# Optimization experiments

Measured on AMD Instinct MI355X. Metric: run time of the kernel, lower is better.

The kernel has to match this reference:

```python
import jax, jax.numpy as jnp
import numpy as np

TAU = 1.0  # gumbel-softmax temperature (torch default arg temperature=1.0)
EPS = 1e-7


def setup_inputs() -> dict:
    key = jax.random.key(0)
    kx, kg, kc, kw = jax.random.split(key, 4)
    B, T, D = 8, 4096, 1024
    G, N = 2, 320
    Cd = D // G  # 512
    x = jax.random.normal(kx, (B, T, D), dtype=jnp.float32)
    # standard Gumbel(0,1) noise, same distribution torch samples internally
    u = jax.random.uniform(kg, (B, T, G, N), dtype=jnp.float32, minval=1e-6, maxval=1.0 - 1e-6)
    gumbel = -jnp.log(-jnp.log(u))
    # codebook init: uniform(-1/num_codes, 1/num_codes)
    codebook = jax.random.uniform(kc, (G, N, Cd), dtype=jnp.float32, minval=-1.0 / N, maxval=1.0 / N)
    proj_w = jax.random.normal(kw, (D, G * N), dtype=jnp.float32) * (1.0 / np.sqrt(D))
    proj_b = jnp.zeros((G * N,), dtype=jnp.float32)
    return {"x": x, "gumbel": gumbel, "codebook": codebook, "proj_w": proj_w, "proj_b": proj_b}


def reference(x, gumbel, codebook, proj_w, proj_b):
    B, T, D = x.shape
    G, N, Cd = codebook.shape
    # projection to per-group code logits: [B,T,G,N]
    logits = (jnp.einsum('btd,de->bte', x, proj_w) + proj_b).reshape(B, T, G, N)
    # hard gumbel-softmax with straight-through estimator (training path)
    y_soft = jax.nn.softmax((logits + gumbel) / TAU, axis=-1)
    idx = jnp.argmax(y_soft, axis=-1)                     # [B,T,G]
    y_hard = jax.nn.one_hot(idx, N, dtype=y_soft.dtype)   # [B,T,G,N]
    probs = y_hard - jax.lax.stop_gradient(y_soft) + y_soft
    # one-hot gather from codebook, expressed as the original einsum
    quantized = jnp.einsum('btgn,gnd->btgd', probs, codebook).reshape(B, T, D)
    # diversity loss: entropy of average code usage per group
    avg_probs = probs.mean(axis=(0, 1))                    # [G,N]
    diversity_loss = -jnp.sum(avg_probs * jnp.log(avg_probs + EPS)) / G
    return quantized, diversity_loss
```

## Files before the change

kernel.cpp:

```cpp
#include <hip/hip_runtime.h>
#include <math.h>

#define M_ROWS 32768
#define KDIM   1024
#define GN     640
#define NGRP   2
#define NCODES 320
#define CD     512

#define BM 64
#define BK 32
#define NT (KDIM / BK)
#define THREADS 512

#define B_TILE_BYTES (4 * GN * 16)

typedef __attribute__((ext_vector_type(8))) short bf16x8;
typedef __attribute__((ext_vector_type(4))) float f32x4;

__device__ __forceinline__ unsigned short f2bf(float f) {
    unsigned u = __builtin_bit_cast(unsigned, f);
    return (unsigned short)((u + 0x7FFFu + ((u >> 16) & 1u)) >> 16);
}
__device__ __forceinline__ unsigned pk2(float lo, float hi) {
    return (unsigned)f2bf(lo) | ((unsigned)f2bf(hi) << 16);
}

__device__ __forceinline__ void gll16(const void* g, void* l) {
    __builtin_amdgcn_global_load_lds(
        (const __attribute__((address_space(1))) unsigned int*)g,
        (__attribute__((address_space(3))) unsigned int*)l, 16, 0, 0);
}

__global__ __launch_bounds__(256) void wt2_kernel(const float* __restrict__ W,
                                                  unsigned short* __restrict__ Wt2,
                                                  int* __restrict__ counts) {
    const int k = blockIdx.x;
    const int t = k >> 5, ks = (k >> 3) & 3, j = k & 7;
    const size_t obase = (((size_t)t * 4 + ks) * GN) * 8 + j;
    for (int c = threadIdx.x; c < GN; c += 256)
        Wt2[obase + (size_t)c * 8] = f2bf(W[(size_t)k * GN + c]);
    if (k == 0)
        for (int i = threadIdx.x; i < GN; i += 256) counts[i] = 0;
}

__global__ __launch_bounds__(THREADS) void gemm_argmax_gather(
    const float* __restrict__ x,
    const float* __restrict__ gumbel,
    const float* __restrict__ codebook,
    const unsigned short* __restrict__ Wt2,
    const float* __restrict__ bias,
    float* __restrict__ out,
    int* __restrict__ counts)
{
    __shared__ __align__(16) unsigned short Bs[4][GN][8];
    __shared__ __align__(16) float As[BM][BK];
    __shared__ float pv[NGRP][2][BM];
    __shared__ int   pi[NGRP][2][BM];
    __shared__ int   idx_s[NGRP][BM];

    const int tid  = threadIdx.x;
    const int widx = tid >> 6;
    const int lane = tid & 63;
    const int l15  = lane & 15;
    const int l4   = lane >> 4;
    const int wn   = widx & 3;
    const int wm   = widx >> 2;
    const int row0 = blockIdx.x * BM;

    f32x4 acc[2][10];
#pragma unroll
    for (int mf = 0; mf < 2; ++mf)
#pragma unroll
        for (int nf = 0; nf < 10; ++nf) acc[mf][nf] = (f32x4){0.f, 0.f, 0.f, 0.f};

    const char* bsrc = (const char*)Wt2 + (size_t)(widx * 5) * 1024 + (size_t)lane * 16;
    char* BsBase = (char*)&Bs[0][0][0];
    const int arow = widx * 8 + (lane >> 3);
    const int asub = lane & 7;
    const int asg  = ((((asub >> 1) ^ (arow & 3)) << 1) | (asub & 1));
    const char* asrc = (const char*)x + (size_t)(row0 + arow) * (KDIM * 4) + (size_t)asg * 16;
    char* AsBase = (char*)&As[0][0];
    char* adst   = AsBase + widx * 1024;

#pragma unroll
    for (int i = 0; i < 5; ++i)
        gll16(bsrc + i * 1024, BsBase + (widx * 5 + i) * 1024);
    gll16(asrc, adst);
    __syncthreads();

    for (int t = 0; t < NT; ++t) {
        bf16x8 afr[2];
#pragma unroll
        for (int mf = 0; mf < 2; ++mf) {
            const int row = wm * 32 + mf * 16 + l15;
            const int q   = l4 ^ (row & 3);
            const float4* pa = reinterpret_cast<const float4*>(AsBase + row * 128 + q * 32);
            float4 a0 = pa[0], a1 = pa[1];
            union { bf16x8 v; unsigned u[4]; } w;
            w.u[0] = pk2(a0.x, a0.y); w.u[1] = pk2(a0.z, a0.w);
            w.u[2] = pk2(a1.x, a1.y); w.u[3] = pk2(a1.z, a1.w);
            afr[mf] = w.v;
        }
#pragma unroll
        for (int nf = 0; nf < 10; ++nf) {
            bf16x8 bfr = *reinterpret_cast<const bf16x8*>(
                BsBase + ((size_t)l4 * GN + wn * 160 + nf * 16 + l15) * 16);
            acc[0][nf] = __builtin_amdgcn_mfma_f32_16x16x32_bf16(afr[0], bfr, acc[0][nf], 0, 0, 0);
            acc[1][nf] = __builtin_amdgcn_mfma_f32_16x16x32_bf16(afr[1], bfr, acc[1][nf], 0, 0, 0);
        }
        __syncthreads();
        if (t + 1 < NT) {
#pragma unroll
            for (int i = 0; i < 5; ++i)
                gll16(bsrc + (size_t)(t + 1) * B_TILE_BYTES + i * 1024,
                      BsBase + (widx * 5 + i) * 1024);
            gll16(asrc + (size_t)(t + 1) * 128, adst);
        }
        __syncthreads();
    }

#pragma unroll
    for (int mf = 0; mf < 2; ++mf) {
#pragma unroll
        for (int j = 0; j < 4; ++j) {
            const int lr = wm * 32 + mf * 16 + l4 * 4 + j;
            const size_t grow = (size_t)(row0 + lr) * GN;
            float best = -INFINITY;
            int bidx = 0;
#pragma unroll
            for (int nf = 0; nf < 10; ++nf) {
                int c = wn * 160 + nf * 16 + l15;
                float v = acc[mf][nf][j] + bias[c] + gumbel[grow + c];
                if (v > best) { best = v; bidx = c; }
            }
#pragma unroll
            for (int m = 1; m < 16; m <<= 1) {
                float ov = __shfl_xor(best, m, 64);
                int   oi = __shfl_xor(bidx, m, 64);
                if (ov > best || (ov == best && oi < bidx)) { best = ov; bidx = oi; }
            }
            if (l15 == 0) {
                pv[wn >> 1][wn & 1][lr] = best;
                pi[wn >> 1][wn & 1][lr] = bidx;
            }
        }
    }
    __syncthreads();

    if (tid < NGRP * BM) {
        const int g = tid >> 6, lr = tid & 63;
        float v0 = pv[g][0][lr], v1 = pv[g][1][lr];
        int   i0 = pi[g][0][lr], i1 = pi[g][1][lr];
        int bi = (v1 > v0) ? i1 : i0;
        int n  = bi - g * NCODES;
        idx_s[g][lr] = n;
        atomicAdd(&counts[g * NCODES + n], 1);
    }
    __syncthreads();

#pragma unroll
    for (int s = 0; s < 32; ++s) {
        int fi = tid + THREADS * s;
        int lr = fi >> 8;
        int q  = fi & 255;
        int g  = q >> 7;
        int n  = idx_s[g][lr];
        float4 cv = *reinterpret_cast<const float4*>(
            &codebook[((size_t)g * NCODES + n) * CD + (q & 127) * 4]);
        *reinterpret_cast<float4*>(&out[(size_t)(row0 + lr) * KDIM + q * 4]) = cv;
    }
}

__global__ void loss_kernel(const int* __restrict__ counts, float* __restrict__ out_loss) {
    __shared__ float red[256];
    float sum = 0.0f;
    for (int i = threadIdx.x; i < GN; i += 256) {
        float avg = (float)counts[i] * (1.0f / (float)M_ROWS);
        sum += avg * logf(avg + 1e-7f);
    }
    red[threadIdx.x] = sum;
    __syncthreads();
    for (int s = 128; s > 0; s >>= 1) {
        if (threadIdx.x < s) red[threadIdx.x] += red[threadIdx.x + s];
        __syncthreads();
    }
    if (threadIdx.x == 0) out_loss[0] = -red[0] * (1.0f / (float)NGRP);
}

extern "C" void kernel_launch(void* const* d_in, const int* in_sizes, int n_in,
                              void* d_out, int out_size, void* d_ws, size_t ws_size,
                              hipStream_t stream) {
    const float* x        = (const float*)d_in[0];
    const float* gumbel   = (const float*)d_in[1];
    const float* codebook = (const float*)d_in[2];
    const float* W        = (const float*)d_in[3];
    const float* bias     = (const float*)d_in[4];
    float* out = (float*)d_out;

    unsigned short* Wt2 = (unsigned short*)d_ws;
    int* counts = (int*)((char*)d_ws + (size_t)GN * KDIM * 2 + 256);

    wt2_kernel<<<dim3(KDIM), dim3(256), 0, stream>>>(W, Wt2, counts);
    gemm_argmax_gather<<<dim3(M_ROWS / BM), dim3(THREADS), 0, stream>>>(
        x, gumbel, codebook, Wt2, bias, out, counts);
    loss_kernel<<<dim3(1), dim3(256), 0, stream>>>(
        counts, out + (size_t)M_ROWS * KDIM);
}
```

Baseline: 126.2 us.

## Split GEMM across column quarters with atomicMax argmax keys and separate gather

Each block now computes a 64-row by 160-column quarter of the logits instead of all 640 columns. The partial argmax results are combined through 64-bit atomicMax keys that pack an order-preserving float with an inverted index. The codebook gather and usage counting move into a separate kernel. The GEMM now double-buffers B in LDS, prefetches A straight into registers, and swizzles block IDs for XCD locality. The intent is more parallelism and lower per-block register/LDS use, at the cost of reading x four times, an extra kernel launch, and global atomics.

```diff
diff --git a/kernel.cpp b/kernel.cpp
--- a/kernel.cpp
+++ b/kernel.cpp
@@ -11,9 +11,10 @@
 #define BM 64
 #define BK 32
 #define NT (KDIM / BK)
-#define THREADS 512
-
-#define B_TILE_BYTES (4 * GN * 16)
+#define QBN 160
+#define NQ 4
+#define QSLAB 10240
+#define THREADS 256
 
 typedef __attribute__((ext_vector_type(8))) short bf16x8;
 typedef __attribute__((ext_vector_type(4))) float f32x4;
@@ -25,150 +26,148 @@
 __device__ __forceinline__ unsigned pk2(float lo, float hi) {
     return (unsigned)f2bf(lo) | ((unsigned)f2bf(hi) << 16);
 }
-
 __device__ __forceinline__ void gll16(const void* g, void* l) {
     __builtin_amdgcn_global_load_lds(
         (const __attribute__((address_space(1))) unsigned int*)g,
         (__attribute__((address_space(3))) unsigned int*)l, 16, 0, 0);
 }
 
-__global__ __launch_bounds__(256) void wt2_kernel(const float* __restrict__ W,
-                                                  unsigned short* __restrict__ Wt2,
-                                                  int* __restrict__ counts) {
+__global__ __launch_bounds__(256) void prep_kernel(const float* __restrict__ W,
+                                                   unsigned short* __restrict__ Wt3,
+                                                   unsigned long long* __restrict__ keys,
+                                                   int* __restrict__ counts) {
     const int k = blockIdx.x;
     const int t = k >> 5, ks = (k >> 3) & 3, j = k & 7;
-    const size_t obase = (((size_t)t * 4 + ks) * GN) * 8 + j;
-    for (int c = threadIdx.x; c < GN; c += 256)
-        Wt2[obase + (size_t)c * 8] = f2bf(W[(size_t)k * GN + c]);
-    if (k == 0)
+    for (int c = threadIdx.x; c < GN; c += 256) {
+        int qq = c / QBN, cl = c % QBN;
+        Wt3[((((size_t)t * NQ + qq) * 4 + ks) * QBN + cl) * 8 + j] =
+            f2bf(W[(size_t)k * GN + c]);
+    }
+    int gtid = blockIdx.x * 256 + threadIdx.x;
+    if (gtid < M_ROWS * NGRP) keys[gtid] = 0ull;
+    if (blockIdx.x == 0)
         for (int i = threadIdx.x; i < GN; i += 256) counts[i] = 0;
 }
 
-__global__ __launch_bounds__(THREADS) void gemm_argmax_gather(
+__global__ __launch_bounds__(THREADS) void gemm_argmax(
     const float* __restrict__ x,
     const float* __restrict__ gumbel,
-    const float* __restrict__ codebook,
-    const unsigned short* __restrict__ Wt2,
+    const unsigned short* __restrict__ Wt3,
     const float* __restrict__ bias,
-    float* __restrict__ out,
-    int* __restrict__ counts)
+    unsigned long long* __restrict__ keys)
 {
-    __shared__ __align__(16) unsigned short Bs[4][GN][8];
-    __shared__ __align__(16) float As[BM][BK];
-    __shared__ float pv[NGRP][2][BM];
-    __shared__ int   pi[NGRP][2][BM];
-    __shared__ int   idx_s[NGRP][BM];
+    __shared__ __align__(16) unsigned short Bs[2][4][QBN][8];
 
     const int tid  = threadIdx.x;
-    const int widx = tid >> 6;
+    const int wid  = tid >> 6;
     const int lane = tid & 63;
     const int l15  = lane & 15;
     const int l4   = lane >> 4;
-    const int wn   = widx & 3;
-    const int wm   = widx >> 2;
-    const int row0 = blockIdx.x * BM;
-
-    f32x4 acc[2][10];
-#pragma unroll
-    for (int mf = 0; mf < 2; ++mf)
-#pragma unroll
-        for (int nf = 0; nf < 10; ++nf) acc[mf][nf] = (f32x4){0.f, 0.f, 0.f, 0.f};
-
-    const char* bsrc = (const char*)Wt2 + (size_t)(widx * 5) * 1024 + (size_t)lane * 16;
-    char* BsBase = (char*)&Bs[0][0][0];
-    const int arow = widx * 8 + (lane >> 3);
-    const int asub = lane & 7;
-    const int asg  = ((((asub >> 1) ^ (arow & 3)) << 1) | (asub & 1));
-    const char* asrc = (const char*)x + (size_t)(row0 + arow) * (KDIM * 4) + (size_t)asg * 16;
-    char* AsBase = (char*)&As[0][0];
-    char* adst   = AsBase + widx * 1024;
-
-#pragma unroll
-    for (int i = 0; i < 5; ++i)
-        gll16(bsrc + i * 1024, BsBase + (widx * 5 + i) * 1024);
-    gll16(asrc, adst);
+
+    const int b   = blockIdx.x;
+    const int xcd = b & 7;
+    const int l   = b >> 3;
+    const int qq  = l & 3;
+    const int rt  = xcd * 64 + (l >> 2);
+    const int row0 = rt * BM;
+
+    f32x4 acc[10];
+#pragma unroll
+    for (int nf = 0; nf < 10; ++nf) acc[nf] = (f32x4){0.f, 0.f, 0.f, 0.f};
+
+    const float* aptr = x + (size_t)(row0 + wid * 16 + l15) * KDIM + l4 * 8;
+    const char* bsrc = (const char*)Wt3 + (size_t)qq * QSLAB + (size_t)lane * 16;
+    char* BsB = (char*)&Bs[0][0][0][0];
+
+    for (int s = wid; s < 10; s += 4)
+        gll16(bsrc + s * 1024, BsB + s * 1024);
+    float4 a0 = *reinterpret_cast<const float4*>(aptr);
+    float4 a1 = *reinterpret_cast<const float4*>(aptr + 4);
     __syncthreads();
 
     for (int t = 0; t < NT; ++t) {
-        bf16x8 afr[2];
-#pragma unroll
-        for (int mf = 0; mf < 2; ++mf) {
-            const int row = wm * 32 + mf * 16 + l15;
-            const int q   = l4 ^ (row & 3);
-            const float4* pa = reinterpret_cast<const float4*>(AsBase + row * 128 + q * 32);
-            float4 a0 = pa[0], a1 = pa[1];
-            union { bf16x8 v; unsigned u[4]; } w;
-            w.u[0] = pk2(a0.x, a0.y); w.u[1] = pk2(a0.z, a0.w);
-            w.u[2] = pk2(a1.x, a1.y); w.u[3] = pk2(a1.z, a1.w);
-            afr[mf] = w.v;
-        }
+        const int buf = t & 1;
+        float4 n0, n1;
+        if (t + 1 < NT) {
+            for (int s = wid; s < 10; s += 4)
+                gll16(bsrc + (size_t)(t + 1) * (NQ * QSLAB) + s * 1024,
+                      BsB + (buf ^ 1) * QSLAB + s * 1024);
+            n0 = *reinterpret_cast<const float4*>(aptr + (t + 1) * BK);
+            n1 = *reinterpret_cast<const float4*>(aptr + (t + 1) * BK + 4);
+        }
+        union { bf16x8 v; unsigned u[4]; } w;
+        w.u[0] = pk2(a0.x, a0.y); w.u[1] = pk2(a0.z, a0.w);
+        w.u[2] = pk2(a1.x, a1.y); w.u[3] = pk2(a1.z, a1.w);
+        bf16x8 af = w.v;
 #pragma unroll
         for (int nf = 0; nf < 10; ++nf) {
             bf16x8 bfr = *reinterpret_cast<const bf16x8*>(
-                BsBase + ((size_t)l4 * GN + wn * 160 + nf * 16 + l15) * 16);
-            acc[0][nf] = __builtin_amdgcn_mfma_f32_16x16x32_bf16(afr[0], bfr, acc[0][nf], 0, 0, 0);
-            acc[1][nf] = __builtin_amdgcn_mfma_f32_16x16x32_bf16(afr[1], bfr, acc[1][nf], 0, 0, 0);
-        }
+                BsB + buf * QSLAB + ((l4 * QBN + nf * 16 + l15) * 16));
+            acc[nf] = __builtin_amdgcn_mfma_f32_16x16x32_bf16(af, bfr, acc[nf], 0, 0, 0);
+        }
+        if (t + 1 < NT) { a0 = n0; a1 = n1; }
         __syncthreads();
-        if (t + 1 < NT) {
-#pragma unroll
-            for (int i = 0; i < 5; ++i)
-                gll16(bsrc + (size_t)(t + 1) * B_TILE_BYTES + i * 1024,
-                      BsBase + (widx * 5 + i) * 1024);
-            gll16(asrc + (size_t)(t + 1) * 128, adst);
-        }
-        __syncthreads();
-    }
-
-#pragma unroll
-    for (int mf = 0; mf < 2; ++mf) {
-#pragma unroll
-        for (int j = 0; j < 4; ++j) {
-            const int lr = wm * 32 + mf * 16 + l4 * 4 + j;
-            const size_t grow = (size_t)(row0 + lr) * GN;
-            float best = -INFINITY;
-            int bidx = 0;
-#pragma unroll
-            for (int nf = 0; nf < 10; ++nf) {
-                int c = wn * 160 + nf * 16 + l15;
-                float v = acc[mf][nf][j] + bias[c] + gumbel[grow + c];
-                if (v > best) { best = v; bidx = c; }
-            }
-#pragma unroll
-            for (int m = 1; m < 16; m <<= 1) {
-                float ov = __shfl_xor(best, m, 64);
-                int   oi = __shfl_xor(bidx, m, 64);
-                if (ov > best || (ov == best && oi < bidx)) { best = ov; bidx = oi; }
-            }
-            if (l15 == 0) {
-                pv[wn >> 1][wn & 1][lr] = best;
-                pi[wn >> 1][wn & 1][lr] = bidx;
-            }
-        }
+    }
+
+    float bv[10];
+#pragma unroll
+    for (int nf = 0; nf < 10; ++nf) bv[nf] = bias[qq * QBN + nf * 16 + l15];
+    const int g     = qq >> 1;
+    const int nbase = (qq & 1) * QBN;
+#pragma unroll
+    for (int j = 0; j < 4; ++j) {
+        const int lr = wid * 16 + l4 * 4 + j;
+        const size_t r = row0 + lr;
+        float best = -INFINITY;
+        int bn = 0;
+#pragma unroll
+        for (int nf = 0; nf < 10; ++nf) {
+            int n = nbase + nf * 16 + l15;
+            float v = acc[nf][j] + bv[nf] + gumbel[r * GN + g * NCODES + n];
+            if (v > best) { best = v; bn = n; }
+        }
+#pragma unroll
+        for (int m = 1; m < 16; m <<= 1) {
+            float ov = __shfl_xor(best, m, 64);
+            int   on = __shfl_xor(bn, m, 64);
+            if (ov > best || (ov == best && on < bn)) { best = ov; bn = on; }
+        }
+        if (l15 == 0) {
+            unsigned ub = __builtin_bit_cast(unsigned, best);
+            unsigned su = (ub & 0x80000000u) ? ~ub : (ub | 0x80000000u);
+            unsigned long long key =
+                ((unsigned long long)su << 32) | (unsigned)(NCODES - 1 - bn);
+            atomicMax(&keys[r * NGRP + g], key);
+        }
+    }
+}
+
+__global__ __launch_bounds__(256) void gather_kernel(
+    const unsigned long long* __restrict__ keys,
+    const float* __restrict__ codebook,
+    int* __restrict__ counts,
+    float* __restrict__ out)
+{
+    __shared__ int ns[8][2];
+    const int t  = threadIdx.x;
+    const int rb = blockIdx.x * 8;
+    if (t < 16) {
+        int lr = t >> 1, g = t & 1;
+        unsigned long long key = keys[(size_t)(rb + lr) * NGRP + g];
+        int n = NCODES - 1 - (int)(key & 0xFFFFFFFFull);
+        ns[lr][g] = n;
+        atomicAdd(&counts[g * NCODES + n], 1);
     }
     __syncthreads();
-
-    if (tid < NGRP * BM) {
-        const int g = tid >> 6, lr = tid & 63;
-        float v0 = pv[g][0][lr], v1 = pv[g][1][lr];
-        int   i0 = pi[g][0][lr], i1 = pi[g][1][lr];
-        int bi = (v1 > v0) ? i1 : i0;
-        int n  = bi - g * NCODES;
-        idx_s[g][lr] = n;
-        atomicAdd(&counts[g * NCODES + n], 1);
-    }
-    __syncthreads();
-
-#pragma unroll
-    for (int s = 0; s < 32; ++s) {
-        int fi = tid + THREADS * s;
-        int lr = fi >> 8;
-        int q  = fi & 255;
-        int g  = q >> 7;
-        int n  = idx_s[g][lr];
+#pragma unroll
+    for (int s = 0; s < 8; ++s) {
+        int fi = t + 256 * s;
+        int lr = fi >> 8, q = fi & 255;
+        int g = q >> 7, d4 = q & 127;
+        int n = ns[lr][g];
         float4 cv = *reinterpret_cast<const float4*>(
-            &codebook[((size_t)g * NCODES + n) * CD + (q & 127) * 4]);
-        *reinterpret_cast<float4*>(&out[(size_t)(row0 + lr) * KDIM + q * 4]) = cv;
+            &codebook[((size_t)g * NCODES + n) * CD + d4 * 4]);
+        *reinterpret_cast<float4*>(&out[(size_t)(rb + lr) * KDIM + q * 4]) = cv;
     }
 }
 
@@ -198,12 +197,15 @@
     const float* bias     = (const float*)d_in[4];
     float* out = (float*)d_out;
 
-    unsigned short* Wt2 = (unsigned short*)d_ws;
-    int* counts = (int*)((char*)d_ws + (size_t)GN * KDIM * 2 + 256);
-
-    wt2_kernel<<<dim3(KDIM), dim3(256), 0, stream>>>(W, Wt2, counts);
-    gemm_argmax_gather<<<dim3(M_ROWS / BM), dim3(THREADS), 0, stream>>>(
-        x, gumbel, codebook, Wt2, bias, out, counts);
+    unsigned short* Wt3 = (unsigned short*)d_ws;
+    unsigned long long* keys = (unsigned long long*)((char*)d_ws + 1310720);
+    int* counts = (int*)((char*)d_ws + 1310720 + 524288);
+
+    prep_kernel<<<dim3(KDIM), dim3(256), 0, stream>>>(W, Wt3, keys, counts);
+    gemm_argmax<<<dim3(2048), dim3(THREADS), 0, stream>>>(
+        x, gumbel, Wt3, bias, keys);
+    gather_kernel<<<dim3(M_ROWS / 8), dim3(256), 0, stream>>>(
+        keys, codebook, counts, out);
     loss_kernel<<<dim3(1), dim3(256), 0, stream>>>(
         counts, out + (size_t)M_ROWS * KDIM);
 }
```

Result: slower. 162.0 us (+28.4%).

## Split GEMM blocks per codebook group and load A directly into registers

Applied to the files above, without the earlier changes.

Each block now handles one 64-row tile for a single codebook group, giving 1024 blocks of 256 threads instead of 512 blocks of 512 threads. Block indices are remapped so that tiles sharing rows sit on the same XCD. The weight matrix is re-laid out per group into contiguous slabs, so the B fragments become a straight lane-indexed LDS read. The A operand now goes from global memory into registers and is prefetched one step ahead, with no LDS staging. The cost is that every x row is loaded twice, once per group, and the A reads are now uncoalesced strided register loads rather than LDS staging.

```diff
diff --git a/kernel.cpp b/kernel.cpp
--- a/kernel.cpp
+++ b/kernel.cpp
@@ -11,9 +11,8 @@
 #define BM 64
 #define BK 32
 #define NT (KDIM / BK)
-#define THREADS 512
-
-#define B_TILE_BYTES (4 * GN * 16)
+#define THREADS 256
+#define SLAB 20480
 
 typedef __attribute__((ext_vector_type(8))) short bf16x8;
 typedef __attribute__((ext_vector_type(4))) float f32x4;
@@ -25,48 +24,56 @@
 __device__ __forceinline__ unsigned pk2(float lo, float hi) {
     return (unsigned)f2bf(lo) | ((unsigned)f2bf(hi) << 16);
 }
-
 __device__ __forceinline__ void gll16(const void* g, void* l) {
     __builtin_amdgcn_global_load_lds(
         (const __attribute__((address_space(1))) unsigned int*)g,
         (__attribute__((address_space(3))) unsigned int*)l, 16, 0, 0);
 }
 
-__global__ __launch_bounds__(256) void wt2_kernel(const float* __restrict__ W,
-                                                  unsigned short* __restrict__ Wt2,
-                                                  int* __restrict__ counts) {
+__global__ __launch_bounds__(256) void prep_kernel(const float* __restrict__ W,
+                                                   unsigned short* __restrict__ Wt4,
+                                                   int* __restrict__ counts) {
     const int k = blockIdx.x;
     const int t = k >> 5, ks = (k >> 3) & 3, j = k & 7;
-    const size_t obase = (((size_t)t * 4 + ks) * GN) * 8 + j;
-    for (int c = threadIdx.x; c < GN; c += 256)
-        Wt2[obase + (size_t)c * 8] = f2bf(W[(size_t)k * GN + c]);
-    if (k == 0)
+    for (int c = threadIdx.x; c < GN; c += 256) {
+        int g   = c / NCODES;
+        int cl  = c % NCODES;
+        int c16 = cl >> 4, cm = cl & 15;
+        size_t idx = (size_t)(t * 2 + g) * 10240 + c16 * 512 + (ks * 16 + cm) * 8 + j;
+        Wt4[idx] = f2bf(W[(size_t)k * GN + c]);
+    }
+    if (blockIdx.x == 0)
         for (int i = threadIdx.x; i < GN; i += 256) counts[i] = 0;
 }
 
-__global__ __launch_bounds__(THREADS) void gemm_argmax_gather(
+__global__ __launch_bounds__(THREADS) void gemm_fused(
     const float* __restrict__ x,
     const float* __restrict__ gumbel,
     const float* __restrict__ codebook,
-    const unsigned short* __restrict__ Wt2,
+    const unsigned short* __restrict__ Wt4,
     const float* __restrict__ bias,
     float* __restrict__ out,
     int* __restrict__ counts)
 {
-    __shared__ __align__(16) unsigned short Bs[4][GN][8];
-    __shared__ __align__(16) float As[BM][BK];
-    __shared__ float pv[NGRP][2][BM];
-    __shared__ int   pi[NGRP][2][BM];
-    __shared__ int   idx_s[NGRP][BM];
+    __shared__ __align__(16) char Bs[SLAB];
+    __shared__ float pv[2][BM];
+    __shared__ int   pi[2][BM];
+    __shared__ int   idx_s[BM];
 
     const int tid  = threadIdx.x;
-    const int widx = tid >> 6;
+    const int wid  = tid >> 6;
     const int lane = tid & 63;
     const int l15  = lane & 15;
     const int l4   = lane >> 4;
-    const int wn   = widx & 3;
-    const int wm   = widx >> 2;
-    const int row0 = blockIdx.x * BM;
+    const int wn   = wid & 1;
+    const int wm   = wid >> 1;
+
+    const int b    = blockIdx.x;
+    const int xcd  = b & 7;
+    const int q    = b >> 3;
+    const int g    = q & 1;
+    const int rt   = xcd * 64 + (q >> 1);
+    const int row0 = rt * BM;
 
     f32x4 acc[2][10];
 #pragma unroll
@@ -74,50 +81,65 @@
 #pragma unroll
         for (int nf = 0; nf < 10; ++nf) acc[mf][nf] = (f32x4){0.f, 0.f, 0.f, 0.f};
 
-    const char* bsrc = (const char*)Wt2 + (size_t)(widx * 5) * 1024 + (size_t)lane * 16;
-    char* BsBase = (char*)&Bs[0][0][0];
-    const int arow = widx * 8 + (lane >> 3);
-    const int asub = lane & 7;
-    const int asg  = ((((asub >> 1) ^ (arow & 3)) << 1) | (asub & 1));
-    const char* asrc = (const char*)x + (size_t)(row0 + arow) * (KDIM * 4) + (size_t)asg * 16;
-    char* AsBase = (char*)&As[0][0];
-    char* adst   = AsBase + widx * 1024;
-
-#pragma unroll
-    for (int i = 0; i < 5; ++i)
-        gll16(bsrc + i * 1024, BsBase + (widx * 5 + i) * 1024);
-    gll16(asrc, adst);
+    const float* ap0 = x + (size_t)(row0 + wm * 32 + l15) * KDIM + l4 * 8;
+    const float* ap1 = ap0 + 16 * KDIM;
+    const char* bsrc0 = (const char*)Wt4 + (size_t)g * SLAB + wid * 5120 + (size_t)lane * 16;
+
+#define STAGE_B(t) do {                                                 \
+        const char* s_ = bsrc0 + (size_t)(t) * (2 * SLAB);              \
+        char* d_ = Bs + wid * 5120;                                     \
+        gll16(s_,        d_);                                           \
+        gll16(s_ + 1024, d_ + 1024);                                    \
+        gll16(s_ + 2048, d_ + 2048);                                    \
+        gll16(s_ + 3072, d_ + 3072);                                    \
+        gll16(s_ + 4096, d_ + 4096);                                    \
+    } while (0)
+
+#define LOAD_A(t, dst) do {                                             \
+        const float* p0_ = ap0 + (size_t)(t) * BK;                      \
+        const float* p1_ = ap1 + (size_t)(t) * BK;                      \
+        dst[0] = *reinterpret_cast<const float4*>(p0_);                 \
+        dst[1] = *reinterpret_cast<const float4*>(p0_ + 4);             \
+        dst[2] = *reinterpret_cast<const float4*>(p1_);                 \
+        dst[3] = *reinterpret_cast<const float4*>(p1_ + 4);             \
+    } while (0)
+
+#define CONV_A(src, a0_, a1_) do {                                      \
+        union { bf16x8 v; unsigned u[4]; } w0_, w1_;                    \
+        w0_.u[0] = pk2(src[0].x, src[0].y);                             \
+        w0_.u[1] = pk2(src[0].z, src[0].w);                             \
+        w0_.u[2] = pk2(src[1].x, src[1].y);                             \
+        w0_.u[3] = pk2(src[1].z, src[1].w);                             \
+        w1_.u[0] = pk2(src[2].x, src[2].y);                             \
+        w1_.u[1] = pk2(src[2].z, src[2].w);                             \
+        w1_.u[2] = pk2(src[3].x, src[3].y);                             \
+        w1_.u[3] = pk2(src[3].z, src[3].w);                             \
+        a0_ = w0_.v; a1_ = w1_.v;                                       \
+    } while (0)
+
+    float4 nx[4];
+    bf16x8 af0, af1;
+    STAGE_B(0);
+    LOAD_A(0, nx);
+    CONV_A(nx, af0, af1);
     __syncthreads();
 
     for (int t = 0; t < NT; ++t) {
-        bf16x8 afr[2];
-#pragma unroll
-        for (int mf = 0; mf < 2; ++mf) {
-            const int row = wm * 32 + mf * 16 + l15;
-            const int q   = l4 ^ (row & 3);
-            const float4* pa = reinterpret_cast<const float4*>(AsBase + row * 128 + q * 32);
-            float4 a0 = pa[0], a1 = pa[1];
-            union { bf16x8 v; unsigned u[4]; } w;
-            w.u[0] = pk2(a0.x, a0.y); w.u[1] = pk2(a0.z, a0.w);
-            w.u[2] = pk2(a1.x, a1.y); w.u[3] = pk2(a1.z, a1.w);
-            afr[mf] = w.v;
-        }
+        if (t + 1 < NT) LOAD_A(t + 1, nx);
+        const char* bb = Bs + wn * 10240;
 #pragma unroll
         for (int nf = 0; nf < 10; ++nf) {
             bf16x8 bfr = *reinterpret_cast<const bf16x8*>(
-                BsBase + ((size_t)l4 * GN + wn * 160 + nf * 16 + l15) * 16);
-            acc[0][nf] = __builtin_amdgcn_mfma_f32_16x16x32_bf16(afr[0], bfr, acc[0][nf], 0, 0, 0);
-            acc[1][nf] = __builtin_amdgcn_mfma_f32_16x16x32_bf16(afr[1], bfr, acc[1][nf], 0, 0, 0);
+                bb + nf * 1024 + (size_t)lane * 16);
+            acc[0][nf] = __builtin_amdgcn_mfma_f32_16x16x32_bf16(af0, bfr, acc[0][nf], 0, 0, 0);
+            acc[1][nf] = __builtin_amdgcn_mfma_f32_16x16x32_bf16(af1, bfr, acc[1][nf], 0, 0, 0);
         }
-        __syncthreads();
         if (t + 1 < NT) {
-#pragma unroll
-            for (int i = 0; i < 5; ++i)
-                gll16(bsrc + (size_t)(t + 1) * B_TILE_BYTES + i * 1024,
-                      BsBase + (widx * 5 + i) * 1024);
-            gll16(asrc + (size_t)(t + 1) * 128, adst);
+            __syncthreads();
+            STAGE_B(t + 1);
+            CONV_A(nx, af0, af1);
+            __syncthreads();
         }
-        __syncthreads();
     }
 
 #pragma unroll
@@ -125,36 +147,32 @@
 #pragma unroll
         for (int j = 0; j < 4; ++j) {
             const int lr = wm * 32 + mf * 16 + l4 * 4 + j;
-            const size_t grow = (size_t)(row0 + lr) * GN;
+            const size_t r = row0 + lr;
+            const float* grow = gumbel + r * GN + g * NCODES;
+            const float* brow = bias + g * NCODES;
             float best = -INFINITY;
-            int bidx = 0;
+            int bn = 0;
 #pragma unroll
             for (int nf = 0; nf < 10; ++nf) {
-                int c = wn * 160 + nf * 16 + l15;
-                float v = acc[mf][nf][j] + bias[c] + gumbel[grow + c];
-                if (v > best) { best = v; bidx = c; }
+                int n = wn * 160 + nf * 16 + l15;
+                float v = acc[mf][nf][j] + brow[n] + grow[n];
+                if (v > best) { best = v; bn = n; }
             }
 #pragma unroll
             for (int m = 1; m < 16; m <<= 1) {
                 float ov = __shfl_xor(best, m, 64);
-                int   oi = __shfl_xor(bidx, m, 64);
-                if (ov > best || (ov == best && oi < bidx)) { best = ov; bidx = oi; }
+                int   on = __shfl_xor(bn, m, 64);
+                if (ov > best || (ov == best && on < bn)) { best = ov; bn = on; }
             }
-            if (l15 == 0) {
-                pv[wn >> 1][wn & 1][lr] = best;
-                pi[wn >> 1][wn & 1][lr] = bidx;
-            }
+            if (l15 == 0) { pv[wn][lr] = best; pi[wn][lr] = bn; }
         }
     }
     __syncthreads();
 
-    if (tid < NGRP * BM) {
-        const int g = tid >> 6, lr = tid & 63;
-        float v0 = pv[g][0][lr], v1 = pv[g][1][lr];
-        int   i0 = pi[g][0][lr], i1 = pi[g][1][lr];
-        int bi = (v1 > v0) ? i1 : i0;
-        int n  = bi - g * NCODES;
-        idx_s[g][lr] = n;
+    if (tid < BM) {
+        float v0 = pv[0][tid], v1 = pv[1][tid];
+        int n = (v1 > v0) ? pi[1][tid] : pi[0][tid];
+        idx_s[tid] = n;
         atomicAdd(&counts[g * NCODES + n], 1);
     }
     __syncthreads();
@@ -162,14 +180,17 @@
 #pragma unroll
     for (int s = 0; s < 32; ++s) {
         int fi = tid + THREADS * s;
-        int lr = fi >> 8;
-        int q  = fi & 255;
-        int g  = q >> 7;
-        int n  = idx_s[g][lr];
+        int lr = fi >> 7;
+        int d4 = fi & 127;
+        int n  = idx_s[lr];
         float4 cv = *reinterpret_cast<const float4*>(
-            &codebook[((size_t)g * NCODES + n) * CD + (q & 127) * 4]);
-        *reinterpret_cast<float4*>(&out[(size_t)(row0 + lr) * KDIM + q * 4]) = cv;
-    }
+            &codebook[((size_t)g * NCODES + n) * CD + d4 * 4]);
+        *reinterpret_cast<float4*>(
+            &out[(size_t)(row0 + lr) * KDIM + (size_t)g * CD + d4 * 4]) = cv;
+    }
+#undef STAGE_B
+#undef LOAD_A
+#undef CONV_A
 }
 
 __global__ void loss_kernel(const int* __restrict__ counts, float* __restrict__ out_loss) {
@@ -198,12 +219,12 @@
     const float* bias     = (const float*)d_in[4];
     float* out = (float*)d_out;
 
-    unsigned short* Wt2 = (unsigned short*)d_ws;
-    int* counts = (int*)((char*)d_ws + (size_t)GN * KDIM * 2 + 256);
-
-    wt2_kernel<<<dim3(KDIM), dim3(256), 0, stream>>>(W, Wt2, counts);
-    gemm_argmax_gather<<<dim3(M_ROWS / BM), dim3(THREADS), 0, stream>>>(
-        x, gumbel, codebook, Wt2, bias, out, counts);
+    unsigned short* Wt4 = (unsigned short*)d_ws;
+    int* counts = (int*)((char*)d_ws + 1310720 + 256);
+
+    prep_kernel<<<dim3(KDIM), dim3(256), 0, stream>>>(W, Wt4, counts);
+    gemm_fused<<<dim3(1024), dim3(THREADS), 0, stream>>>(
+        x, gumbel, codebook, Wt4, bias, out, counts);
     loss_kernel<<<dim3(1), dim3(256), 0, stream>>>(
         counts, out + (size_t)M_ROWS * KDIM);
 }
```

After: 172.0 us. 36.4% more time.
